# Performance work log

Hardware: AMD Instinct MI355X
Metric: run time of the kernel (lower is better)

## Reference

```python
import jax, jax.numpy as jnp
import numpy as np

NUM_CHANNELS = 512
B_DIM = 64
C_DIM = 16
N = 512
FEAT = NUM_CHANNELS * 4 * 4  # 8192


def setup_inputs() -> dict:
    key = jax.random.key(0)
    k1, k2 = jax.random.split(key)
    inp = jax.random.normal(k1, (N, NUM_CHANNELS, 4, 4), dtype=jnp.float32)
    T = jax.random.normal(k2, (FEAT, B_DIM * C_DIM), dtype=jnp.float32) * 0.1
    return {"inp": inp, "T": T}


def reference(inp, T):
    x = inp.reshape(-1, FEAT)                      # (N, 8192)
    M = (x @ T).reshape(-1, B_DIM, C_DIM)          # (N, B, C)
    # pairwise L1 distance over C: (N, N, B)
    dist = jnp.sum(jnp.abs(M[:, None, :, :] - M[None, :, :, :]), axis=-1)
    o = jnp.sum(jnp.exp(-dist), axis=1)            # (N, B)
    return jnp.concatenate((x, o), axis=1)         # (N, 8192 + B)
```

## Files before the change

kernel.cpp:

```cpp
#include <hip/hip_runtime.h>

#define NROWS 512
#define FEAT  8192
#define BDIM  64
#define CDIM  16
#define MCOLS 1024
#define OUTC  8256
#define KSPLIT 8
#define KCHUNK (FEAT / KSPLIT)
#define MSIZE  (NROWS * MCOLS)

typedef __bf16 bf16x8 __attribute__((ext_vector_type(8)));
typedef float  floatx4 __attribute__((ext_vector_type(4)));
typedef _Float16 half2 __attribute__((ext_vector_type(2)));

#define AS1 __attribute__((address_space(1)))
#define AS3 __attribute__((address_space(3)))

static __device__ __forceinline__ void gload16(const void* g, void* l) {
    __builtin_amdgcn_global_load_lds((AS1 void*)(g), (AS3 void*)(l), 16, 0, 0);
}

static __device__ __forceinline__ unsigned short f2bf(float f) {
    unsigned int x = __builtin_bit_cast(unsigned int, f);
    unsigned int r = (x + 0x7FFFu + ((x >> 16) & 1u)) >> 16;
    return (unsigned short)r;
}

static __device__ __forceinline__ unsigned int pk2h(float a, float b) {
    return __builtin_bit_cast(unsigned int, __builtin_amdgcn_cvt_pkrtz(a, b));
}

static __device__ __forceinline__ half2 absdiff2(unsigned int a, unsigned int b) {
    half2 d = __builtin_bit_cast(half2, a) - __builtin_bit_cast(half2, b);
    return __builtin_bit_cast(half2, __builtin_bit_cast(unsigned int, d) & 0x7FFF7FFFu);
}

__global__ __launch_bounds__(512, 2) void k_prep(const float* __restrict__ x,
                                                 const float* __restrict__ T,
                                                 unsigned short* __restrict__ xb,
                                                 unsigned short* __restrict__ Tt,
                                                 float* __restrict__ out) {
    __shared__ __align__(16) float lds[2][64][65];
    int bid = blockIdx.x, t = threadIdx.x;
    if (bid < 256) {
#pragma unroll
        for (int u = 0; u < 8; ++u) {
            int gid = bid * 4096 + u * 512 + t;
            float4 v = *(const float4*)(x + (size_t)gid * 4);
            ushort4 uu;
            uu.x = f2bf(v.x); uu.y = f2bf(v.y); uu.z = f2bf(v.z); uu.w = f2bf(v.w);
            *(ushort4*)(xb + (size_t)gid * 4) = uu;
            int row = gid >> 11, col4 = gid & 2047;
            *(float4*)(out + (size_t)row * OUTC + col4 * 4) = v;
        }
    } else {
        int b2 = bid - 256;
        int sub = t >> 8, tt = t & 255;
        for (int u = 0; u < 4; ++u) {
            int tile = b2 * 8 + u * 2 + sub;
            int kt = tile & 127, nt = tile >> 7;
            __syncthreads();
            int kk = tt >> 2, q = tt & 3;
#pragma unroll
            for (int p = 0; p < 4; ++p) {
                int c4 = q + p * 4;
                float4 v = *(const float4*)(T + (size_t)(kt * 64 + kk) * MCOLS + nt * 64 + c4 * 4);
                lds[sub][kk][c4 * 4 + 0] = v.x; lds[sub][kk][c4 * 4 + 1] = v.y;
                lds[sub][kk][c4 * 4 + 2] = v.z; lds[sub][kk][c4 * 4 + 3] = v.w;
            }
            __syncthreads();
            int nr = tt >> 2, ck = tt & 3;
            unsigned int wv[8];
#pragma unroll
            for (int j = 0; j < 8; ++j) {
                unsigned int lo = f2bf(lds[sub][ck * 16 + j * 2 + 0][nr]);
                unsigned int hi = f2bf(lds[sub][ck * 16 + j * 2 + 1][nr]);
                wv[j] = lo | (hi << 16);
            }
            uint4* dst = (uint4*)(Tt + (size_t)(nt * 64 + nr) * FEAT + kt * 64 + ck * 16);
            dst[0] = make_uint4(wv[0], wv[1], wv[2], wv[3]);
            dst[1] = make_uint4(wv[4], wv[5], wv[6], wv[7]);
        }
    }
}

__global__ __launch_bounds__(256, 2) void k_gemm(const unsigned short* __restrict__ xb,
                                                 const unsigned short* __restrict__ Tt,
                                                 float* __restrict__ Mp) {
    __shared__ __align__(16) unsigned short ldsA[128 * 64];
    __shared__ __align__(16) unsigned short ldsB[64 * 64];
    int bid = blockIdx.x, t = threadIdx.x;
    int mt = bid & 3, nt = (bid >> 2) & 15, ks = bid >> 6;
    int m0 = mt * 128, n0 = nt * 64, kbase = ks * KCHUNK;
    int w = t >> 6, l = t & 63;

    int c  = (l & 3) ^ ((l >> 3) & 3);
    int lr = l >> 2;
    const unsigned short* gA0 = xb + (size_t)(m0 + w * 32 + lr) * FEAT + kbase + c * 8;
    const unsigned short* gA1 = gA0 + (size_t)16 * FEAT;
    const unsigned short* gB0 = Tt + (size_t)(n0 + w * 16 + lr) * FEAT + kbase + c * 8;
    unsigned short* lA00 = ldsA + (4 * w + 0) * 512;
    unsigned short* lA01 = ldsA + (4 * w + 1) * 512;
    unsigned short* lA10 = ldsA + (4 * w + 2) * 512;
    unsigned short* lA11 = ldsA + (4 * w + 3) * 512;
    unsigned short* lB0  = ldsB + (2 * w + 0) * 512;
    unsigned short* lB1  = ldsB + (2 * w + 1) * 512;

    int wr = w >> 1, wc = w & 1, fm = l & 15, fq = l >> 4;
    int fo = fm * 32 + ((fq ^ ((fm >> 1) & 3)) * 8);
    const unsigned short* paB = ldsA + (wr * 8) * 512 + fo;
    const unsigned short* pbB = ldsB + (wc * 4) * 512 + fo;

    floatx4 acc[4][2] = {};

    for (int kk = 0; kk < KCHUNK; kk += 64) {
        __syncthreads();
        gload16(gA0 + kk,      lA00);
        gload16(gA0 + kk + 32, lA01);
        gload16(gA1 + kk,      lA10);
        gload16(gA1 + kk + 32, lA11);
        gload16(gB0 + kk,      lB0);
        gload16(gB0 + kk + 32, lB1);
        __syncthreads();
#pragma unroll
        for (int h = 0; h < 2; ++h) {
            bf16x8 af[4], bfr[2];
#pragma unroll
            for (int a = 0; a < 4; ++a) af[a]  = *(const bf16x8*)(paB + (a * 2 + h) * 512);
#pragma unroll
            for (int b = 0; b < 2; ++b) bfr[b] = *(const bf16x8*)(pbB + (b * 2 + h) * 512);
#pragma unroll
            for (int a = 0; a < 4; ++a)
#pragma unroll
                for (int b = 0; b < 2; ++b)
                    acc[a][b] = __builtin_amdgcn_mfma_f32_16x16x32_bf16(af[a], bfr[b], acc[a][b], 0, 0, 0);
        }
    }

    float* outp = Mp + (size_t)ks * MSIZE;
    int gr0 = m0 + wr * 64, gc0 = n0 + wc * 32;
#pragma unroll
    for (int a = 0; a < 4; ++a)
#pragma unroll
        for (int r = 0; r < 4; ++r) {
            int row = gr0 + a * 16 + fq * 4 + r;
#pragma unroll
            for (int b = 0; b < 2; ++b)
                outp[(size_t)row * MCOLS + gc0 + b * 16 + fm] = acc[a][b][r];
        }
}

__global__ __launch_bounds__(512, 2) void k_pair(const float* __restrict__ Mp,
                                                 float* __restrict__ out) {
    __shared__ __align__(16) unsigned int ldsMh[NROWS * 12];
    __shared__ float partial[8][64];
    int bid = blockIdx.x, t = threadIdx.x;
    int b = bid & 63, itp = bid >> 6;
#pragma unroll
    for (int p = 0; p < 4; ++p) {
        int idx = t + p * 512;
        int j = idx >> 2, c4 = idx & 3;
        const float* base = Mp + (size_t)j * MCOLS + b * CDIM + c4 * 4;
        float4 s = *(const float4*)base;
#pragma unroll
        for (int k = 1; k < KSPLIT; ++k) {
            float4 v = *(const float4*)(base + (size_t)k * MSIZE);
            s.x += v.x; s.y += v.y; s.z += v.z; s.w += v.w;
        }
        uint2 wv;
        wv.x = pk2h(s.x, s.y);
        wv.y = pk2h(s.z, s.w);
        *(uint2*)&ldsMh[j * 12 + c4 * 2] = wv;
    }
    __syncthreads();

    int lane = t & 63, w = t >> 6, g = t >> 8, wg = (t >> 6) & 3;
    int i = (itp * 2 + g) * 64 + lane;
    uint4 miA = *(const uint4*)&ldsMh[i * 12];
    uint4 miB = *(const uint4*)&ldsMh[i * 12 + 4];

    float acc = 0.0f;
    for (int jj = wg * 128; jj < wg * 128 + 128; ++jj) {
        uint4 mjA = *(const uint4*)&ldsMh[jj * 12];
        uint4 mjB = *(const uint4*)&ldsMh[jj * 12 + 4];
        half2 sA = (absdiff2(miA.x, mjA.x) + absdiff2(miA.y, mjA.y)) +
                   (absdiff2(miA.z, mjA.z) + absdiff2(miA.w, mjA.w));
        half2 sB = (absdiff2(miB.x, mjB.x) + absdiff2(miB.y, mjB.y)) +
                   (absdiff2(miB.z, mjB.z) + absdiff2(miB.w, mjB.w));
        half2 s = sA + sB;
        float d = (float)s.x + (float)s.y;
        acc += __expf(-d);
    }
    partial[w][lane] = acc;
    __syncthreads();
    if ((t & 255) < 64) {
        int ii = (itp * 2 + g) * 64 + (t & 63);
        float o = partial[g * 4 + 0][t & 63] + partial[g * 4 + 1][t & 63] +
                  partial[g * 4 + 2][t & 63] + partial[g * 4 + 3][t & 63];
        out[(size_t)ii * OUTC + FEAT + b] = o;
    }
}

extern "C" void kernel_launch(void* const* d_in, const int* in_sizes, int n_in,
                              void* d_out, int out_size, void* d_ws, size_t ws_size,
                              hipStream_t stream) {
    const float* x = (const float*)d_in[0];
    const float* T = (const float*)d_in[1];
    float* out = (float*)d_out;

    unsigned short* xb = (unsigned short*)d_ws;
    unsigned short* Tt = (unsigned short*)((char*)d_ws + (8u << 20));
    float*          Mp = (float*)((char*)d_ws + (24u << 20));

    k_prep<<<512, 512, 0, stream>>>(x, T, xb, Tt, out);
    k_gemm<<<512, 256, 0, stream>>>(xb, Tt, Mp);
    k_pair<<<256, 512, 0, stream>>>(Mp, out);
}
```

Measured before the change: 137.9 us.

## Fuse bf16 conversion into GEMM loads and move x copy into pair kernel

Removes the separate prep kernel. The GEMM now reads fp32 x and T directly, truncates them to bf16 in registers with a byte permute, and writes the swizzled LDS tiles, prefetching the next k-slice into registers. The passthrough copy of x into the output moves into the pairwise kernel. This saves a launch and the round trip of the bf16 and transposed copies through memory. In exchange the GEMM reads twice the bytes, B is loaded as strided scalar loads, and rounding changes from round-to-nearest to truncation.

```diff
diff --git a/kernel.cpp b/kernel.cpp
--- a/kernel.cpp
+++ b/kernel.cpp
@@ -14,17 +14,9 @@
 typedef float  floatx4 __attribute__((ext_vector_type(4)));
 typedef _Float16 half2 __attribute__((ext_vector_type(2)));
 
-#define AS1 __attribute__((address_space(1)))
-#define AS3 __attribute__((address_space(3)))
-
-static __device__ __forceinline__ void gload16(const void* g, void* l) {
-    __builtin_amdgcn_global_load_lds((AS1 void*)(g), (AS3 void*)(l), 16, 0, 0);
-}
-
-static __device__ __forceinline__ unsigned short f2bf(float f) {
-    unsigned int x = __builtin_bit_cast(unsigned int, f);
-    unsigned int r = (x + 0x7FFFu + ((x >> 16) & 1u)) >> 16;
-    return (unsigned short)r;
+static __device__ __forceinline__ unsigned int pkbf(float lo, float hi) {
+    return __builtin_amdgcn_perm(__builtin_bit_cast(unsigned int, hi),
+                                 __builtin_bit_cast(unsigned int, lo), 0x07060302u);
 }
 
 static __device__ __forceinline__ unsigned int pk2h(float a, float b) {
@@ -36,58 +28,9 @@
     return __builtin_bit_cast(half2, __builtin_bit_cast(unsigned int, d) & 0x7FFF7FFFu);
 }
 
-__global__ __launch_bounds__(512, 2) void k_prep(const float* __restrict__ x,
-                                                 const float* __restrict__ T,
-                                                 unsigned short* __restrict__ xb,
-                                                 unsigned short* __restrict__ Tt,
-                                                 float* __restrict__ out) {
-    __shared__ __align__(16) float lds[2][64][65];
-    int bid = blockIdx.x, t = threadIdx.x;
-    if (bid < 256) {
-#pragma unroll
-        for (int u = 0; u < 8; ++u) {
-            int gid = bid * 4096 + u * 512 + t;
-            float4 v = *(const float4*)(x + (size_t)gid * 4);
-            ushort4 uu;
-            uu.x = f2bf(v.x); uu.y = f2bf(v.y); uu.z = f2bf(v.z); uu.w = f2bf(v.w);
-            *(ushort4*)(xb + (size_t)gid * 4) = uu;
-            int row = gid >> 11, col4 = gid & 2047;
-            *(float4*)(out + (size_t)row * OUTC + col4 * 4) = v;
-        }
-    } else {
-        int b2 = bid - 256;
-        int sub = t >> 8, tt = t & 255;
-        for (int u = 0; u < 4; ++u) {
-            int tile = b2 * 8 + u * 2 + sub;
-            int kt = tile & 127, nt = tile >> 7;
-            __syncthreads();
-            int kk = tt >> 2, q = tt & 3;
-#pragma unroll
-            for (int p = 0; p < 4; ++p) {
-                int c4 = q + p * 4;
-                float4 v = *(const float4*)(T + (size_t)(kt * 64 + kk) * MCOLS + nt * 64 + c4 * 4);
-                lds[sub][kk][c4 * 4 + 0] = v.x; lds[sub][kk][c4 * 4 + 1] = v.y;
-                lds[sub][kk][c4 * 4 + 2] = v.z; lds[sub][kk][c4 * 4 + 3] = v.w;
-            }
-            __syncthreads();
-            int nr = tt >> 2, ck = tt & 3;
-            unsigned int wv[8];
-#pragma unroll
-            for (int j = 0; j < 8; ++j) {
-                unsigned int lo = f2bf(lds[sub][ck * 16 + j * 2 + 0][nr]);
-                unsigned int hi = f2bf(lds[sub][ck * 16 + j * 2 + 1][nr]);
-                wv[j] = lo | (hi << 16);
-            }
-            uint4* dst = (uint4*)(Tt + (size_t)(nt * 64 + nr) * FEAT + kt * 64 + ck * 16);
-            dst[0] = make_uint4(wv[0], wv[1], wv[2], wv[3]);
-            dst[1] = make_uint4(wv[4], wv[5], wv[6], wv[7]);
-        }
-    }
-}
-
-__global__ __launch_bounds__(256, 2) void k_gemm(const unsigned short* __restrict__ xb,
-                                                 const unsigned short* __restrict__ Tt,
-                                                 float* __restrict__ Mp) {
+__global__ __launch_bounds__(256, 2) void k_gemm2(const float* __restrict__ x,
+                                                  const float* __restrict__ T,
+                                                  float* __restrict__ Mp) {
     __shared__ __align__(16) unsigned short ldsA[128 * 64];
     __shared__ __align__(16) unsigned short ldsB[64 * 64];
     int bid = blockIdx.x, t = threadIdx.x;
@@ -95,17 +38,27 @@
     int m0 = mt * 128, n0 = nt * 64, kbase = ks * KCHUNK;
     int w = t >> 6, l = t & 63;
 
-    int c  = (l & 3) ^ ((l >> 3) & 3);
-    int lr = l >> 2;
-    const unsigned short* gA0 = xb + (size_t)(m0 + w * 32 + lr) * FEAT + kbase + c * 8;
-    const unsigned short* gA1 = gA0 + (size_t)16 * FEAT;
-    const unsigned short* gB0 = Tt + (size_t)(n0 + w * 16 + lr) * FEAT + kbase + c * 8;
-    unsigned short* lA00 = ldsA + (4 * w + 0) * 512;
-    unsigned short* lA01 = ldsA + (4 * w + 1) * 512;
-    unsigned short* lA10 = ldsA + (4 * w + 2) * 512;
-    unsigned short* lA11 = ldsA + (4 * w + 3) * 512;
-    unsigned short* lB0  = ldsB + (2 * w + 0) * 512;
-    unsigned short* lB1  = ldsB + (2 * w + 1) * 512;
+    const float* gA[4];
+    unsigned short* lA[4];
+#pragma unroll
+    for (int i = 0; i < 4; ++i) {
+        int q = t + 256 * i, row = q >> 3, cc = q & 7;
+        gA[i] = x + (size_t)(m0 + row) * FEAT + kbase + cc * 8;
+        int r = row & 15;
+        lA[i] = ldsA + (((row >> 4) * 2 + (cc >> 2)) * 512 + r * 32 +
+                        (((cc & 3) ^ ((r >> 1) & 3)) * 8));
+    }
+    const float* gB[2];
+    unsigned short* lB[2];
+    int nr = t & 63;
+#pragma unroll
+    for (int i = 0; i < 2; ++i) {
+        int cc = (t >> 6) + 4 * i;
+        gB[i] = T + (size_t)(kbase + cc * 8) * MCOLS + n0 + nr;
+        int r = nr & 15;
+        lB[i] = ldsB + (((nr >> 4) * 2 + (cc >> 2)) * 512 + r * 32 +
+                        (((cc & 3) ^ ((r >> 1) & 3)) * 8));
+    }
 
     int wr = w >> 1, wc = w & 1, fm = l & 15, fq = l >> 4;
     int fo = fm * 32 + ((fq ^ ((fm >> 1) & 3)) * 8);
@@ -113,16 +66,51 @@
     const unsigned short* pbB = ldsB + (wc * 4) * 512 + fo;
 
     floatx4 acc[4][2] = {};
+    float4 ra[4][2];
+    float  rb[2][8];
+
+#pragma unroll
+    for (int i = 0; i < 4; ++i) {
+        ra[i][0] = *(const float4*)(gA[i]);
+        ra[i][1] = *(const float4*)(gA[i] + 4);
+        gA[i] += 64;
+    }
+#pragma unroll
+    for (int i = 0; i < 2; ++i) {
+#pragma unroll
+        for (int j = 0; j < 8; ++j) rb[i][j] = gB[i][(size_t)j * MCOLS];
+        gB[i] += (size_t)64 * MCOLS;
+    }
 
     for (int kk = 0; kk < KCHUNK; kk += 64) {
         __syncthreads();
-        gload16(gA0 + kk,      lA00);
-        gload16(gA0 + kk + 32, lA01);
-        gload16(gA1 + kk,      lA10);
-        gload16(gA1 + kk + 32, lA11);
-        gload16(gB0 + kk,      lB0);
-        gload16(gB0 + kk + 32, lB1);
+#pragma unroll
+        for (int i = 0; i < 4; ++i)
+            *(uint4*)lA[i] = make_uint4(pkbf(ra[i][0].x, ra[i][0].y),
+                                        pkbf(ra[i][0].z, ra[i][0].w),
+                                        pkbf(ra[i][1].x, ra[i][1].y),
+                                        pkbf(ra[i][1].z, ra[i][1].w));
+#pragma unroll
+        for (int i = 0; i < 2; ++i)
+            *(uint4*)lB[i] = make_uint4(pkbf(rb[i][0], rb[i][1]),
+                                        pkbf(rb[i][2], rb[i][3]),
+                                        pkbf(rb[i][4], rb[i][5]),
+                                        pkbf(rb[i][6], rb[i][7]));
         __syncthreads();
+        if (kk + 64 < KCHUNK) {
+#pragma unroll
+            for (int i = 0; i < 4; ++i) {
+                ra[i][0] = *(const float4*)(gA[i]);
+                ra[i][1] = *(const float4*)(gA[i] + 4);
+                gA[i] += 64;
+            }
+#pragma unroll
+            for (int i = 0; i < 2; ++i) {
+#pragma unroll
+                for (int j = 0; j < 8; ++j) rb[i][j] = gB[i][(size_t)j * MCOLS];
+                gB[i] += (size_t)64 * MCOLS;
+            }
+        }
 #pragma unroll
         for (int h = 0; h < 2; ++h) {
             bf16x8 af[4], bfr[2];
@@ -151,12 +139,22 @@
         }
 }
 
-__global__ __launch_bounds__(512, 2) void k_pair(const float* __restrict__ Mp,
-                                                 float* __restrict__ out) {
+__global__ __launch_bounds__(512, 2) void k_pair2(const float* __restrict__ Mp,
+                                                  const float* __restrict__ x,
+                                                  float* __restrict__ out) {
     __shared__ __align__(16) unsigned int ldsMh[NROWS * 12];
     __shared__ float partial[8][64];
     int bid = blockIdx.x, t = threadIdx.x;
     int b = bid & 63, itp = bid >> 6;
+
+#pragma unroll
+    for (int u = 0; u < 8; ++u) {
+        int gid = bid * 4096 + u * 512 + t;
+        float4 v = *(const float4*)(x + (size_t)gid * 4);
+        int row = gid >> 11, col4 = gid & 2047;
+        *(float4*)(out + (size_t)row * OUTC + col4 * 4) = v;
+    }
+
 #pragma unroll
     for (int p = 0; p < 4; ++p) {
         int idx = t + p * 512;
@@ -209,11 +207,8 @@
     const float* T = (const float*)d_in[1];
     float* out = (float*)d_out;
 
-    unsigned short* xb = (unsigned short*)d_ws;
-    unsigned short* Tt = (unsigned short*)((char*)d_ws + (8u << 20));
-    float*          Mp = (float*)((char*)d_ws + (24u << 20));
-
-    k_prep<<<512, 512, 0, stream>>>(x, T, xb, Tt, out);
-    k_gemm<<<512, 256, 0, stream>>>(xb, Tt, Mp);
-    k_pair<<<256, 512, 0, stream>>>(Mp, out);
-}
+    float* Mp = (float*)d_ws;
+
+    k_gemm2<<<512, 256, 0, stream>>>(x, T, Mp);
+    k_pair2<<<256, 512, 0, stream>>>(Mp, x, out);
+}
```

Result: no change. 140.6 us (+2.0%).
